# Performance work log

Measured on AMD Instinct MI355X. Metric: run time of the kernel, lower is better.

The kernel has to match this reference:

```python
import jax, jax.numpy as jnp
import numpy as np

DIM = 1024
NUM_HEADS = 16
HEAD_DIM = DIM // NUM_HEADS
EPS_NORM = 1e-12  # F.normalize eps
EPS_LN = 1e-5     # nn.LayerNorm eps


def setup_inputs() -> dict:
    key = jax.random.key(0)
    ks = jax.random.split(key, 6)
    x = jax.random.normal(ks[0], (4, 2048, DIM), dtype=jnp.float32)
    # LayerNorm params
    ln_w = jnp.ones((DIM,), jnp.float32)
    ln_b = jnp.zeros((DIM,), jnp.float32)
    # qkv: xavier_uniform on weight [3D, D], zero bias
    limit = float(np.sqrt(6.0 / (DIM + 3 * DIM)))
    qkv_w = jax.random.uniform(ks[1], (3 * DIM, DIM), jnp.float32, -limit, limit)
    qkv_b = jnp.zeros((3 * DIM,), jnp.float32)
    # out_proj: normal std=0.02, zero bias
    out_w = 0.02 * jax.random.normal(ks[2], (DIM, DIM), dtype=jnp.float32)
    out_b = jnp.zeros((DIM,), jnp.float32)
    return {"x": x, "ln_w": ln_w, "ln_b": ln_b, "qkv_w": qkv_w,
            "qkv_b": qkv_b, "out_w": out_w, "out_b": out_b}


def reference(x, ln_w, ln_b, qkv_w, qkv_b, out_w, out_b):
    B, N, D = x.shape
    # pre-LayerNorm
    mu = jnp.mean(x, axis=-1, keepdims=True)
    var = jnp.mean(jnp.square(x - mu), axis=-1, keepdims=True)
    h = (x - mu) / jnp.sqrt(var + EPS_LN) * ln_w + ln_b
    # QKV projection (torch Linear: y = h @ W^T + b)
    qkv = h @ qkv_w.T + qkv_b                     # [B, N, 3D]
    qkv = qkv.reshape(B, N, 3, NUM_HEADS, HEAD_DIM)
    q, k, v = (jnp.transpose(qkv[:, :, i], (0, 2, 1, 3)) for i in range(3))  # [B,H,N,hd]
    # per-head L2 normalize (F.normalize semantics: x / max(||x||, eps))
    q = q / jnp.maximum(jnp.linalg.norm(q, axis=-1, keepdims=True), EPS_NORM)
    k = k / jnp.maximum(jnp.linalg.norm(k, axis=-1, keepdims=True), EPS_NORM)
    scale = HEAD_DIM ** 0.5
    attn = jnp.einsum('bhqd,bhkd->bhqk', q, k) * scale
    attn = jax.nn.softmax(attn, axis=-1)
    out = jnp.einsum('bhqk,bhkd->bhqd', attn, v)  # [B,H,N,hd]
    out = jnp.transpose(out, (0, 2, 1, 3)).reshape(B, N, D)
    return x + out @ out_w.T + out_b
```

## Files before the change

kernel.cpp:

```cpp
#include <hip/hip_runtime.h>
#include <math.h>

constexpr int D     = 1024;
constexpr int NH    = 16;
constexpr int HD    = 64;
constexpr int SEQ   = 2048;
constexpr int BATCH = 4;
constexpr int NTOK  = BATCH * SEQ;

typedef short s16x8 __attribute__((ext_vector_type(8)));
typedef short s16x4 __attribute__((ext_vector_type(4)));
typedef float f32x4 __attribute__((ext_vector_type(4)));
typedef unsigned short u16;
typedef unsigned int   u32;

#if __has_builtin(__builtin_amdgcn_exp2f)
#define EXP2(x) __builtin_amdgcn_exp2f(x)
#else
#define EXP2(x) exp2f(x)
#endif

__device__ __forceinline__ short f2bf(float f) {
    unsigned u = __float_as_uint(f);
    unsigned r = (u + 0x7FFFu + ((u >> 16) & 1u)) >> 16;
    return (short)r;
}
__device__ __forceinline__ float bf2f(u16 s) {
    return __uint_as_float(((unsigned)s) << 16);
}

__device__ __forceinline__ u32 pack_bf16_pair(float f0, float f1) {
    u32 a = __float_as_uint(f1) + 0x8000u;
    u32 b = __float_as_uint(f0) + 0x8000u;
    return __builtin_amdgcn_perm(a, b, 0x07060302u);
}

__device__ __forceinline__ void async_lds16(const void* g, void* l) {
    __builtin_amdgcn_global_load_lds(
        (const __attribute__((address_space(1))) unsigned int*)g,
        (__attribute__((address_space(3))) unsigned int*)l, 16, 0, 0);
}

__device__ __forceinline__ float block_reduce_sum(float v, float* red) {
    int lane = threadIdx.x & 63, wid = threadIdx.x >> 6;
    #pragma unroll
    for (int off = 32; off > 0; off >>= 1) v += __shfl_down(v, off, 64);
    if (lane == 0) red[wid] = v;
    __syncthreads();
    float r = red[0] + red[1] + red[2] + red[3];
    __syncthreads();
    return r;
}

__global__ __launch_bounds__(256) void ln_kernel(const float* __restrict__ x,
                                                 const float* __restrict__ w,
                                                 const float* __restrict__ b,
                                                 u16* __restrict__ h) {
    __shared__ float red[4];
    int row = blockIdx.x;
    const float* xr = x + (size_t)row * D;
    int t = threadIdx.x;
    float v[4];
    float s = 0.f;
    #pragma unroll
    for (int i = 0; i < 4; i++) { v[i] = xr[t + 256 * i]; s += v[i]; }
    float mean = block_reduce_sum(s, red) * (1.0f / 1024.0f);
    float ss = 0.f;
    #pragma unroll
    for (int i = 0; i < 4; i++) { float d = v[i] - mean; ss += d * d; }
    float var = block_reduce_sum(ss, red) * (1.0f / 1024.0f);
    float rstd = rsqrtf(var + 1e-5f);
    u16* hr = h + (size_t)row * D;
    #pragma unroll
    for (int i = 0; i < 4; i++) {
        int c = t + 256 * i;
        hr[c] = (u16)f2bf((v[i] - mean) * rstd * w[c] + b[c]);
    }
}

__global__ __launch_bounds__(256) void cast_kernel(const float* __restrict__ in,
                                                   u16* __restrict__ out, int n) {
    int i = (blockIdx.x * 256 + threadIdx.x) * 4;
    if (i >= n) return;
    float4 f = *(const float4*)(in + i);
    s16x4 o4;
    o4[0] = f2bf(f.x); o4[1] = f2bf(f.y); o4[2] = f2bf(f.z); o4[3] = f2bf(f.w);
    *(s16x4*)(out + i) = o4;
}

template <typename OutT, bool RES>
__global__ __launch_bounds__(256) void gemm_bf16(const u16* __restrict__ A,
                                                 const u16* __restrict__ B,
                                                 const float* __restrict__ bias,
                                                 const float* __restrict__ R,
                                                 OutT* __restrict__ C,
                                                 int M, int N, int K) {
    __shared__ u16 As[128 * 32];
    __shared__ u16 Bs[128 * 32];
    int tid = threadIdx.x, wave = tid >> 6, lane = tid & 63;
    int quad = lane >> 4, l16 = lane & 15;
    int wm = (wave & 1) * 64, wn = (wave >> 1) * 64;
    int rowBase = blockIdx.y * 128, colBase = blockIdx.x * 128;

    int srow = lane >> 2;
    int sk8  = (lane & 3) * 8;

    f32x4 acc[4][4];
    #pragma unroll
    for (int i = 0; i < 4; i++)
        #pragma unroll
        for (int j = 0; j < 4; j++)
            acc[i][j] = (f32x4){0.f, 0.f, 0.f, 0.f};

    for (int k0 = 0; k0 < K; k0 += 32) {
        __syncthreads();
        #pragma unroll
        for (int i = 0; i < 2; i++) {
            int r = wave * 32 + i * 16;
            const u16* ga = A + (size_t)(rowBase + r + srow) * K + k0 + sk8;
            async_lds16(ga, &As[r * 32]);
            const u16* gb = B + (size_t)(colBase + r + srow) * K + k0 + sk8;
            async_lds16(gb, &Bs[r * 32]);
        }
        __syncthreads();

        s16x8 af[4], bfr[4];
        #pragma unroll
        for (int t = 0; t < 4; t++) {
            af[t]  = *(const s16x8*)&As[(wm + t * 16 + l16) * 32 + quad * 8];
            bfr[t] = *(const s16x8*)&Bs[(wn + t * 16 + l16) * 32 + quad * 8];
        }
        #pragma unroll
        for (int mt = 0; mt < 4; mt++)
            #pragma unroll
            for (int nt = 0; nt < 4; nt++)
                acc[mt][nt] = __builtin_amdgcn_mfma_f32_16x16x32_bf16(
                    af[mt], bfr[nt], acc[mt][nt], 0, 0, 0);
    }

    #pragma unroll
    for (int mt = 0; mt < 4; mt++) {
        #pragma unroll
        for (int nt = 0; nt < 4; nt++) {
            int gm0 = rowBase + wm + mt * 16 + quad * 4;
            int gn  = colBase + wn + nt * 16 + l16;
            float bv = bias[gn];
            #pragma unroll
            for (int r = 0; r < 4; r++) {
                int gm = gm0 + r;
                float val = acc[mt][nt][r] + bv;
                if (RES) val += R[(size_t)gm * N + gn];
                if constexpr (sizeof(OutT) == 2)
                    C[(size_t)gm * N + gn] = (OutT)f2bf(val);
                else
                    C[(size_t)gm * N + gn] = val;
            }
        }
    }
}

__global__ __launch_bounds__(256) void knorm_kernel(u16* __restrict__ qkv) {
    int gw = (blockIdx.x * 256 + threadIdx.x) >> 6;
    int lane = threadIdx.x & 63;
    int row = gw / NH, hh = gw - row * NH;
    u16* kp = qkv + (size_t)row * 3072 + 1024 + hh * 64;

    float kv = bf2f(kp[lane]);
    float s = kv * kv;
    #pragma unroll
    for (int off = 32; off > 0; off >>= 1) s += __shfl_down(s, off, 64);
    s = __shfl(s, 0, 64);
    kp[lane] = (u16)f2bf(kv / fmaxf(sqrtf(s), 1e-12f));
}

__global__ __launch_bounds__(256) void mha_kernel(const u16* __restrict__ qkv,
                                                  u16* __restrict__ out) {
    constexpr int LDP = 72;
    __shared__ u16 Ks[64][LDP];
    __shared__ u16 Vt[64][LDP];

    int bh = blockIdx.x >> 4;
    int qt = blockIdx.x & 15;
    int b  = bh >> 4, h = bh & 15;
    int tid = threadIdx.x;
    int wave = tid >> 6, lane = tid & 63;
    int quad = lane >> 4, l16 = lane & 15;

    const size_t rs = 3072;
    constexpr float SCL = 11.5415605f;

    s16x8 aq[2][2];
    #pragma unroll
    for (int rt = 0; rt < 2; rt++) {
        const u16* qb = qkv + ((size_t)(b * SEQ) + qt * 128 + wave * 32 + rt * 16 + l16) * rs + h * 64;
        s16x8 r0 = *(const s16x8*)(qb + quad * 8);
        s16x8 r1 = *(const s16x8*)(qb + 32 + quad * 8);
        float f0[8], f1[8], ss = 0.f;
        #pragma unroll
        for (int i = 0; i < 8; i++) { f0[i] = bf2f((u16)r0[i]); ss = fmaf(f0[i], f0[i], ss); }
        #pragma unroll
        for (int i = 0; i < 8; i++) { f1[i] = bf2f((u16)r1[i]); ss = fmaf(f1[i], f1[i], ss); }
        ss += __shfl_xor(ss, 16, 64);
        ss += __shfl_xor(ss, 32, 64);
        float inv = SCL / fmaxf(sqrtf(ss), 1e-12f);
        #pragma unroll
        for (int i = 0; i < 8; i++) {
            aq[rt][0][i] = f2bf(f0[i] * inv);
            aq[rt][1][i] = f2bf(f1[i] * inv);
        }
    }

    const f32x4 cinit = {-SCL, -SCL, -SCL, -SCL};
    f32x4 o2[2][4];
    #pragma unroll
    for (int rt = 0; rt < 2; rt++)
        #pragma unroll
        for (int ht = 0; ht < 4; ht++) o2[rt][ht] = (f32x4){0.f, 0.f, 0.f, 0.f};
    float lsum[2] = {0.f, 0.f};

    int skey = tid >> 2, sseg = (tid & 3) * 16;
    int vp2 = tid >> 3, dc = (tid & 7) * 8;
    const u16* kglob  = qkv + ((size_t)(b * SEQ) + skey) * rs + 1024 + h * 64 + sseg;
    const u16* vglob0 = qkv + ((size_t)(b * SEQ) + 2 * vp2) * rs + 2048 + h * 64 + dc;
    u32* vt32 = (u32*)&Vt[0][0];

    s16x8 kr0 = ((const s16x8*)kglob)[0];
    s16x8 kr1 = ((const s16x8*)kglob)[1];
    s16x8 vr0 = *(const s16x8*)(vglob0);
    s16x8 vr1 = *(const s16x8*)(vglob0 + rs);

    for (int kb = 0; kb < SEQ / 64; kb++) {
        __syncthreads();
        *(s16x8*)&Ks[skey][sseg]     = kr0;
        *(s16x8*)&Ks[skey][sseg + 8] = kr1;
        #pragma unroll
        for (int i = 0; i < 8; i++) {
            u32 pk = (u32)(u16)vr0[i] | ((u32)(u16)vr1[i] << 16);
            vt32[(dc + i) * (LDP / 2) + vp2] = pk;
        }
        __syncthreads();

        if (kb < SEQ / 64 - 1) {
            const u16* kp = kglob + (size_t)(kb + 1) * 64 * rs;
            const u16* vp = vglob0 + (size_t)(kb + 1) * 64 * rs;
            kr0 = ((const s16x8*)kp)[0];
            kr1 = ((const s16x8*)kp)[1];
            vr0 = *(const s16x8*)(vp);
            vr1 = *(const s16x8*)(vp + rs);
        }

        s16x8 bk[4][2];
        #pragma unroll
        for (int t = 0; t < 4; t++) {
            bk[t][0] = *(const s16x8*)&Ks[t * 16 + l16][quad * 8];
            bk[t][1] = *(const s16x8*)&Ks[t * 16 + l16][32 + quad * 8];
        }

        s16x4 pfr[2][4];
        #pragma unroll
        for (int rt = 0; rt < 2; rt++) {
            float sum16 = 0.f;
            #pragma unroll
            for (int t = 0; t < 4; t++) {
                f32x4 s = cinit;
                s = __builtin_amdgcn_mfma_f32_16x16x32_bf16(bk[t][0], aq[rt][0], s, 0, 0, 0);
                s = __builtin_amdgcn_mfma_f32_16x16x32_bf16(bk[t][1], aq[rt][1], s, 0, 0, 0);
                float p0 = EXP2(s[0]);
                float p1 = EXP2(s[1]);
                float p2 = EXP2(s[2]);
                float p3 = EXP2(s[3]);
                sum16 += (p0 + p1) + (p2 + p3);
                uint2 pk2;
                pk2.x = pack_bf16_pair(p0, p1);
                pk2.y = pack_bf16_pair(p2, p3);
                pfr[rt][t] = __builtin_bit_cast(s16x4, pk2);
            }
            sum16 += __shfl_xor(sum16, 16, 64);
            sum16 += __shfl_xor(sum16, 32, 64);
            lsum[rt] += sum16;
        }

        #pragma unroll
        for (int pr = 0; pr < 2; pr++) {
            int tA = pr * 2, tB = pr * 2 + 1;
            #pragma unroll
            for (int ht = 0; ht < 4; ht++) {
                const u16* vrow = &Vt[ht * 16 + l16][0];
                s16x4 va = *(const s16x4*)(vrow + tA * 16 + quad * 4);
                s16x4 vb = *(const s16x4*)(vrow + tB * 16 + quad * 4);
                s16x8 vfr = __builtin_shufflevector(va, vb, 0, 1, 2, 3, 4, 5, 6, 7);
                #pragma unroll
                for (int rt = 0; rt < 2; rt++) {
                    s16x8 bp = __builtin_shufflevector(pfr[rt][tA], pfr[rt][tB],
                                                       0, 1, 2, 3, 4, 5, 6, 7);
                    o2[rt][ht] = __builtin_amdgcn_mfma_f32_16x16x32_bf16(
                        vfr, bp, o2[rt][ht], 0, 0, 0);
                }
            }
        }
    }

    #pragma unroll
    for (int rt = 0; rt < 2; rt++) {
        float inv = 1.0f / lsum[rt];
        int orow = b * SEQ + qt * 128 + wave * 32 + rt * 16 + l16;
        u16* op = out + (size_t)orow * D + h * 64 + quad * 4;
        #pragma unroll
        for (int ht = 0; ht < 4; ht++) {
            f32x4 v = o2[rt][ht];
            u32 lo = pack_bf16_pair(v[0] * inv, v[1] * inv);
            u32 hi = pack_bf16_pair(v[2] * inv, v[3] * inv);
            uint2 pk = {lo, hi};
            *(uint2*)(op + ht * 16) = pk;
        }
    }
}

extern "C" void kernel_launch(void* const* d_in, const int* in_sizes, int n_in,
                              void* d_out, int out_size, void* d_ws, size_t ws_size,
                              hipStream_t stream) {
    const float* x     = (const float*)d_in[0];
    const float* ln_w  = (const float*)d_in[1];
    const float* ln_b  = (const float*)d_in[2];
    const float* qkv_w = (const float*)d_in[3];
    const float* qkv_b = (const float*)d_in[4];
    const float* out_w = (const float*)d_in[5];
    const float* out_b = (const float*)d_in[6];
    float* y = (float*)d_out;

    char* ws = (char*)d_ws;
    u16* qkv = (u16*)ws;
    u16* h   = (u16*)(ws + (size_t)48 * 1024 * 1024);
    u16* wq  = (u16*)(ws + (size_t)64 * 1024 * 1024);
    u16* wo  = (u16*)(ws + (size_t)70 * 1024 * 1024);
    u16* attn_out = h;

    ln_kernel<<<NTOK, 256, 0, stream>>>(x, ln_w, ln_b, h);
    cast_kernel<<<(3 * D * D) / 1024, 256, 0, stream>>>(qkv_w, wq, 3 * D * D);
    cast_kernel<<<(D * D) / 1024, 256, 0, stream>>>(out_w, wo, D * D);

    {
        dim3 grid(3 * D / 128, NTOK / 128);
        gemm_bf16<u16, false><<<grid, 256, 0, stream>>>(h, wq, qkv_b, nullptr, qkv,
                                                        NTOK, 3 * D, D);
    }

    knorm_kernel<<<NTOK * NH / 4, 256, 0, stream>>>(qkv);

    mha_kernel<<<BATCH * NH * (SEQ / 128), 256, 0, stream>>>(qkv, attn_out);

    {
        dim3 grid(D / 128, NTOK / 128);
        gemm_bf16<float, true><<<grid, 256, 0, stream>>>(attn_out, wo, out_b, x, y,
                                                         NTOK, D, D);
    }
}
```

Measured before the change: 340.1 us.

## Double attention query tile per block and swizzle K shared-memory layout

Each attention block now handles 256 queries instead of 128, with each wave owning 64 query rows, so every K/V tile loaded into shared memory is reused across twice as many queries. K is stored unpadded with an XOR swizzle to avoid bank conflicts, and V's transposed padding shrinks from 72 to 68. Launch bounds now request 2 blocks per SM. The grid halves to 512 blocks, and accumulator and register use roughly doubles, which risks lower occupancy or spills.

```diff
diff --git a/kernel.cpp b/kernel.cpp
--- a/kernel.cpp
+++ b/kernel.cpp
@@ -173,14 +173,14 @@
     kp[lane] = (u16)f2bf(kv / fmaxf(sqrtf(s), 1e-12f));
 }
 
-__global__ __launch_bounds__(256) void mha_kernel(const u16* __restrict__ qkv,
-                                                  u16* __restrict__ out) {
-    constexpr int LDP = 72;
-    __shared__ u16 Ks[64][LDP];
-    __shared__ u16 Vt[64][LDP];
-
-    int bh = blockIdx.x >> 4;
-    int qt = blockIdx.x & 15;
+__global__ __launch_bounds__(256, 2) void mha_kernel(const u16* __restrict__ qkv,
+                                                     u16* __restrict__ out) {
+    __shared__ u16 Ks[64 * 64];
+    constexpr int VS = 68;
+    __shared__ u16 Vt[64 * VS];
+
+    int bh = blockIdx.x >> 3;
+    int qt = blockIdx.x & 7;
     int b  = bh >> 4, h = bh & 15;
     int tid = threadIdx.x;
     int wave = tid >> 6, lane = tid & 63;
@@ -189,10 +189,10 @@
     const size_t rs = 3072;
     constexpr float SCL = 11.5415605f;
 
-    s16x8 aq[2][2];
-    #pragma unroll
-    for (int rt = 0; rt < 2; rt++) {
-        const u16* qb = qkv + ((size_t)(b * SEQ) + qt * 128 + wave * 32 + rt * 16 + l16) * rs + h * 64;
+    s16x8 aq[4][2];
+    #pragma unroll
+    for (int rt = 0; rt < 4; rt++) {
+        const u16* qb = qkv + ((size_t)(b * SEQ) + qt * 256 + wave * 64 + rt * 16 + l16) * rs + h * 64;
         s16x8 r0 = *(const s16x8*)(qb + quad * 8);
         s16x8 r1 = *(const s16x8*)(qb + 32 + quad * 8);
         float f0[8], f1[8], ss = 0.f;
@@ -211,32 +211,37 @@
     }
 
     const f32x4 cinit = {-SCL, -SCL, -SCL, -SCL};
-    f32x4 o2[2][4];
-    #pragma unroll
-    for (int rt = 0; rt < 2; rt++)
+    f32x4 o2[4][4];
+    #pragma unroll
+    for (int rt = 0; rt < 4; rt++)
         #pragma unroll
         for (int ht = 0; ht < 4; ht++) o2[rt][ht] = (f32x4){0.f, 0.f, 0.f, 0.f};
-    float lsum[2] = {0.f, 0.f};
-
-    int skey = tid >> 2, sseg = (tid & 3) * 16;
+    float lsum[4] = {0.f, 0.f, 0.f, 0.f};
+
+    int skey = tid >> 2, c4 = tid & 3;
+    int ksw  = skey & 7;
     int vp2 = tid >> 3, dc = (tid & 7) * 8;
-    const u16* kglob  = qkv + ((size_t)(b * SEQ) + skey) * rs + 1024 + h * 64 + sseg;
+    const u16* kglob  = qkv + ((size_t)(b * SEQ) + skey) * rs + 1024 + h * 64 + c4 * 16;
     const u16* vglob0 = qkv + ((size_t)(b * SEQ) + 2 * vp2) * rs + 2048 + h * 64 + dc;
-    u32* vt32 = (u32*)&Vt[0][0];
+    u16* kdst0 = &Ks[skey * 64 + ((2 * c4)     ^ ksw) * 8];
+    u16* kdst1 = &Ks[skey * 64 + ((2 * c4 + 1) ^ ksw) * 8];
+    u32* vt32 = (u32*)&Vt[0];
 
     s16x8 kr0 = ((const s16x8*)kglob)[0];
     s16x8 kr1 = ((const s16x8*)kglob)[1];
     s16x8 vr0 = *(const s16x8*)(vglob0);
     s16x8 vr1 = *(const s16x8*)(vglob0 + rs);
 
+    int swz = l16 & 7;
+
     for (int kb = 0; kb < SEQ / 64; kb++) {
         __syncthreads();
-        *(s16x8*)&Ks[skey][sseg]     = kr0;
-        *(s16x8*)&Ks[skey][sseg + 8] = kr1;
+        *(s16x8*)kdst0 = kr0;
+        *(s16x8*)kdst1 = kr1;
         #pragma unroll
         for (int i = 0; i < 8; i++) {
             u32 pk = (u32)(u16)vr0[i] | ((u32)(u16)vr1[i] << 16);
-            vt32[(dc + i) * (LDP / 2) + vp2] = pk;
+            vt32[(dc + i) * (VS / 2) + vp2] = pk;
         }
         __syncthreads();
 
@@ -249,35 +254,35 @@
             vr1 = *(const s16x8*)(vp + rs);
         }
 
-        s16x8 bk[4][2];
+        s16x4 pfr[4][4];
+        float sum16[4] = {0.f, 0.f, 0.f, 0.f};
         #pragma unroll
         for (int t = 0; t < 4; t++) {
-            bk[t][0] = *(const s16x8*)&Ks[t * 16 + l16][quad * 8];
-            bk[t][1] = *(const s16x8*)&Ks[t * 16 + l16][32 + quad * 8];
-        }
-
-        s16x4 pfr[2][4];
-        #pragma unroll
-        for (int rt = 0; rt < 2; rt++) {
-            float sum16 = 0.f;
+            const u16* krow = &Ks[(t * 16 + l16) * 64];
+            s16x8 bk0 = *(const s16x8*)(krow + ((0 + quad) ^ swz) * 8);
+            s16x8 bk1 = *(const s16x8*)(krow + ((4 + quad) ^ swz) * 8);
             #pragma unroll
-            for (int t = 0; t < 4; t++) {
+            for (int rt = 0; rt < 4; rt++) {
                 f32x4 s = cinit;
-                s = __builtin_amdgcn_mfma_f32_16x16x32_bf16(bk[t][0], aq[rt][0], s, 0, 0, 0);
-                s = __builtin_amdgcn_mfma_f32_16x16x32_bf16(bk[t][1], aq[rt][1], s, 0, 0, 0);
+                s = __builtin_amdgcn_mfma_f32_16x16x32_bf16(bk0, aq[rt][0], s, 0, 0, 0);
+                s = __builtin_amdgcn_mfma_f32_16x16x32_bf16(bk1, aq[rt][1], s, 0, 0, 0);
                 float p0 = EXP2(s[0]);
                 float p1 = EXP2(s[1]);
                 float p2 = EXP2(s[2]);
                 float p3 = EXP2(s[3]);
-                sum16 += (p0 + p1) + (p2 + p3);
+                sum16[rt] += (p0 + p1) + (p2 + p3);
                 uint2 pk2;
                 pk2.x = pack_bf16_pair(p0, p1);
                 pk2.y = pack_bf16_pair(p2, p3);
                 pfr[rt][t] = __builtin_bit_cast(s16x4, pk2);
             }
-            sum16 += __shfl_xor(sum16, 16, 64);
-            sum16 += __shfl_xor(sum16, 32, 64);
-            lsum[rt] += sum16;
+        }
+        #pragma unroll
+        for (int rt = 0; rt < 4; rt++) {
+            float s16v = sum16[rt];
+            s16v += __shfl_xor(s16v, 16, 64);
+            s16v += __shfl_xor(s16v, 32, 64);
+            lsum[rt] += s16v;
         }
 
         #pragma unroll
@@ -285,12 +290,12 @@
             int tA = pr * 2, tB = pr * 2 + 1;
             #pragma unroll
             for (int ht = 0; ht < 4; ht++) {
-                const u16* vrow = &Vt[ht * 16 + l16][0];
+                const u16* vrow = &Vt[(ht * 16 + l16) * VS];
                 s16x4 va = *(const s16x4*)(vrow + tA * 16 + quad * 4);
                 s16x4 vb = *(const s16x4*)(vrow + tB * 16 + quad * 4);
                 s16x8 vfr = __builtin_shufflevector(va, vb, 0, 1, 2, 3, 4, 5, 6, 7);
                 #pragma unroll
-                for (int rt = 0; rt < 2; rt++) {
+                for (int rt = 0; rt < 4; rt++) {
                     s16x8 bp = __builtin_shufflevector(pfr[rt][tA], pfr[rt][tB],
                                                        0, 1, 2, 3, 4, 5, 6, 7);
                     o2[rt][ht] = __builtin_amdgcn_mfma_f32_16x16x32_bf16(
@@ -301,9 +306,9 @@
     }
 
     #pragma unroll
-    for (int rt = 0; rt < 2; rt++) {
+    for (int rt = 0; rt < 4; rt++) {
         float inv = 1.0f / lsum[rt];
-        int orow = b * SEQ + qt * 128 + wave * 32 + rt * 16 + l16;
+        int orow = b * SEQ + qt * 256 + wave * 64 + rt * 16 + l16;
         u16* op = out + (size_t)orow * D + h * 64 + quad * 4;
         #pragma unroll
         for (int ht = 0; ht < 4; ht++) {
@@ -347,7 +352,7 @@
 
     knorm_kernel<<<NTOK * NH / 4, 256, 0, stream>>>(qkv);
 
-    mha_kernel<<<BATCH * NH * (SEQ / 128), 256, 0, stream>>>(qkv, attn_out);
+    mha_kernel<<<BATCH * NH * (SEQ / 256), 256, 0, stream>>>(qkv, attn_out);
 
     {
         dim3 grid(D / 128, NTOK / 128);
```

Result: faster. 312.3 us (-8.2%).
